# Kernel optimization log

Measured on AMD Instinct MI355X. Metric: run time of the kernel, lower is better.

Reference implementation:

```python
import jax, jax.numpy as jnp
import numpy as np

N_WRD = 2000
WCODE = 3
EMB = 32
VSIZE = 7
VIEW = (16, 16)
B = 64
CSIZE = 128


def _vcode():
    # torch.meshgrid with default 'ij' indexing, cat -> (2, H*W) -> (H*W, 2)
    x = jnp.linspace(-1.0, 1.0, VIEW[0])
    y = jnp.linspace(-1.0, 1.0, VIEW[1])
    xg, yg = jnp.meshgrid(x, y, indexing='ij')
    return jnp.stack([xg.reshape(-1), yg.reshape(-1)], axis=-1)  # (V, 2)


def setup_inputs() -> dict:
    key = jax.random.key(0)
    ks = jax.random.split(key, 20)
    s = 0.02
    d = {
        'view_cell': jax.random.normal(ks[0], (B, CSIZE, VIEW[0] * VIEW[1]), jnp.float32),
        'v': jax.random.normal(ks[1], (B, VSIZE), jnp.float32),
        'w2c_w1': jax.random.normal(ks[2], (VSIZE, 512), jnp.float32) * s,
        'w2c_b1': jnp.zeros((512,), jnp.float32),
        'w2c_w2': jax.random.normal(ks[3], (512, WCODE * N_WRD), jnp.float32) * s,
        'w2c_b2': jnp.zeros((WCODE * N_WRD,), jnp.float32),
        'fc1_w': jax.random.normal(ks[4], (WCODE, 256), jnp.float32) * s,
        'fc1_b': jnp.zeros((256,), jnp.float32),
        'fc2_w': jax.random.normal(ks[5], (256, 256), jnp.float32) * s,
        'fc2_b': jnp.zeros((256,), jnp.float32),
        'fca_w': jax.random.normal(ks[6], (256, 1), jnp.float32) * s,
        'fca_b': jnp.zeros((1,), jnp.float32),
        'fce_w': jax.random.normal(ks[7], (256, EMB), jnp.float32) * s,
        'fce_b': jnp.zeros((EMB,), jnp.float32),
        'vse_w1': jax.random.normal(ks[8], (2, 128), jnp.float32) * s,
        'vse_b1': jnp.zeros((128,), jnp.float32),
        'vse_w2': jax.random.normal(ks[9], (128, EMB), jnp.float32) * s,
        'vse_b2': jnp.zeros((EMB,), jnp.float32),
    }
    return d


def reference(view_cell, v, w2c_w1, w2c_b1, w2c_w2, w2c_b2,
              fc1_w, fc1_b, fc2_w, fc2_b, fca_w, fca_b, fce_w, fce_b,
              vse_w1, vse_b1, vse_w2, vse_b2):
    b = v.shape[0]
    # w2c: v -> per-cell world codes
    h0 = jax.nn.relu(v @ w2c_w1 + w2c_b1)                     # (B, 512)
    wcode = (h0 @ w2c_w2 + w2c_b2).reshape(-1, WCODE)          # (B*N, 3)
    h = jax.nn.relu(wcode @ fc1_w + fc1_b)                     # (B*N, 256)
    h = jax.nn.relu(h @ fc2_w + fc2_b)
    activation = jax.nn.sigmoid(h @ fca_w + fca_b).reshape(b, N_WRD, 1)
    cs_emb = (h @ fce_w + fce_b).reshape(b, N_WRD, EMB)        # (B, N, E)
    # view-space embedding of the pixel grid
    vcode = _vcode()                                           # (V, 2)
    vs = jax.nn.relu(vcode @ vse_w1 + vse_b1) @ vse_w2 + vse_b2  # (V, E)
    # relation / gated softmax routing
    relation = jnp.einsum('bne,ve->bnv', cs_emb, vs)           # (B, N, V)
    route = jax.nn.softmax(relation, axis=2) * activation      # (B, N, V)
    # write: view_cell (B, C, V) @ route^T (B, V, N) -> (B, C, N)
    wrd_cell = jnp.einsum('bcv,bnv->bcn', view_cell, route)
    return wrd_cell
```

## Files before the change

### kernel.cpp

```cpp
#include <hip/hip_runtime.h>
#include <hip/hip_bf16.h>
#include <math.h>

#define NWRD 2000
#define BB 64
#define CS 128
#define VV 256

typedef __attribute__((ext_vector_type(8)))  short short8;
typedef __attribute__((ext_vector_type(16))) float f32x16;

#define WS_FC2WT 0
#define WS_WCODE (WS_FC2WT + 32768)
#define WS_VSB   (WS_WCODE + 384000)
#define WS_EMBB  (WS_VSB + 4096)
#define WS_ACT   (WS_EMBB + 2048000)
#define WS_VCB   (WS_ACT + 128000)
#define WS_FCEWT (WS_VCB + 1048576)
#define WS_H0B   (WS_FCEWT + 4096)
#define WS_W2T   WS_EMBB

__device__ __forceinline__ unsigned short f2bf(float x) {
    unsigned int u = __float_as_uint(x);
    u += 0x7fffu + ((u >> 16) & 1u);
    return (unsigned short)(u >> 16);
}

__global__ __launch_bounds__(256) void k0_vcb(const float* __restrict__ vc,
                                              unsigned short* __restrict__ vcb) {
    int i = (blockIdx.x * 256 + threadIdx.x) * 8;
    float4 f0 = *(const float4*)(vc + i);
    float4 f1 = *(const float4*)(vc + i + 4);
    union { short8 v; unsigned short u[8]; } o;
    o.u[0] = f2bf(f0.x); o.u[1] = f2bf(f0.y); o.u[2] = f2bf(f0.z); o.u[3] = f2bf(f0.w);
    o.u[4] = f2bf(f1.x); o.u[5] = f2bf(f1.y); o.u[6] = f2bf(f1.z); o.u[7] = f2bf(f1.w);
    *(short8*)(vcb + i) = o.v;
}

__global__ __launch_bounds__(256) void k0w_fc2t(const float* __restrict__ fc2_w,
                                                unsigned short* __restrict__ fc2wT) {
    __shared__ unsigned short tile[64][72];
    int t = threadIdx.x;
    int k0t = (blockIdx.x >> 2) * 64, n0t = (blockIdx.x & 3) * 64;
    int nl = t & 63, kb = (t >> 6) * 16;
#pragma unroll
    for (int i = 0; i < 16; i++)
        tile[kb + i][nl] = f2bf(fc2_w[(size_t)(k0t + kb + i)*256 + n0t + nl]);
    __syncthreads();
    int kl = t & 63, nb = (t >> 6) * 16;
#pragma unroll
    for (int i = 0; i < 16; i++)
        fc2wT[(size_t)(n0t + nb + i)*256 + k0t + kl] = tile[kl][nb + i];
}

__global__ __launch_bounds__(256) void k0e_fcet(const float* __restrict__ fce_w,
                                                unsigned short* __restrict__ fcewT) {
    int t = threadIdx.x;
    int e = t & 31, kb = (t >> 5) * 32;
    unsigned short tmp[32];
#pragma unroll
    for (int i = 0; i < 32; i++) tmp[i] = f2bf(fce_w[(size_t)(kb + i)*32 + e]);
#pragma unroll
    for (int i = 0; i < 4; i++)
        *(short8*)(fcewT + (size_t)e*256 + kb + i*8) = *(short8*)(tmp + i*8);
}

__global__ void k1_h0(const float* __restrict__ v, const float* __restrict__ w1,
                      const float* __restrict__ b1, unsigned short* __restrict__ h0b) {
    int b = blockIdx.x, j = threadIdx.x;
    float s = b1[j];
#pragma unroll
    for (int k = 0; k < 7; k++) s = fmaf(v[b*7 + k], w1[k*512 + j], s);
    h0b[b*512 + j] = f2bf(fmaxf(s, 0.f));
}

__global__ __launch_bounds__(256) void k2t_w2(const float* __restrict__ w2,
                                              unsigned short* __restrict__ w2T) {
    __shared__ unsigned short tile[64][66];
    int t = threadIdx.x;
    int n0 = blockIdx.x * 64;
    int k0 = blockIdx.y * 64;
    int nl = t & 63, kb = (t >> 6) * 16;
    int nc = (n0 + nl) < 6000 ? (n0 + nl) : 5999;
#pragma unroll
    for (int i = 0; i < 16; i++)
        tile[nl][kb + i] = f2bf(w2[(size_t)(k0 + kb + i)*6000 + nc]);
    __syncthreads();
    int kl = t & 63, nb = (t >> 6) * 16;
#pragma unroll
    for (int i = 0; i < 16; i++) {
        int nn = n0 + nb + i;
        if (nn < 6000) w2T[(size_t)nn*512 + k0 + kl] = tile[nb + i][kl];
    }
}

__global__ __launch_bounds__(512) void k2_gemm(const unsigned short* __restrict__ h0b,
        const unsigned short* __restrict__ w2T, const float* __restrict__ b2,
        float* __restrict__ wcode) {
    int t = threadIdx.x;
    int w = t >> 6, lane = t & 63, l31 = lane & 31, h = lane >> 5;
    int mt = w & 1, nt = w >> 1;
    int n = blockIdx.x*128 + nt*32 + l31;
    int nc = n < 6000 ? n : 5999;
    f32x16 acc;
#pragma unroll
    for (int i = 0; i < 16; i++) acc[i] = 0.f;
#pragma unroll 8
    for (int ks = 0; ks < 32; ks++) {
        int k0 = ks*16 + h*8;
        short8 af = *(const short8*)(h0b + (mt*32 + l31)*512 + k0);
        short8 bf = *(const short8*)(w2T + (size_t)nc*512 + k0);
        acc = __builtin_amdgcn_mfma_f32_32x32x16_bf16(af, bf, acc, 0, 0, 0);
    }
    if (n < 6000) {
        float bias = b2[n];
#pragma unroll
        for (int i = 0; i < 16; i++) {
            int row = (i & 3) + 8*(i >> 2) + 4*h;
            wcode[(size_t)(mt*32 + row)*6000 + n] = acc[i] + bias;
        }
    }
}

__global__ __launch_bounds__(256) void k3_vs(const float* __restrict__ w1,
        const float* __restrict__ b1, const float* __restrict__ w2,
        const float* __restrict__ b2, unsigned short* __restrict__ vsb) {
    __shared__ float hs[8][128];
    int t = threadIdx.x;
    int m = t & 127, half = t >> 7;
#pragma unroll
    for (int q = 0; q < 4; q++) {
        int vloc = half*4 + q;
        int v = blockIdx.x*8 + vloc;
        float x = (2.f/15.f)*(float)(v >> 4) - 1.f;
        float y = (2.f/15.f)*(float)(v & 15) - 1.f;
        float h = b1[m] + x*w1[m] + y*w1[128 + m];
        hs[vloc][m] = fmaxf(h, 0.f);
    }
    __syncthreads();
    int vloc = t >> 5, e = t & 31;
    float s = b2[e];
    for (int mm = 0; mm < 128; mm++) s = fmaf(hs[vloc][mm], w2[mm*32 + e], s);
    vsb[(blockIdx.x*8 + vloc)*32 + e] = f2bf(s);
}

#define K45_LDS 75776
__global__ __launch_bounds__(512, 4) void k45(
        const unsigned short* __restrict__ vcb,
        const float* __restrict__ wcode,
        const float* __restrict__ fc1_w, const float* __restrict__ fc1_b,
        const unsigned short* __restrict__ fc2wT, const float* __restrict__ fc2_b,
        const float* __restrict__ fca_w, const float* __restrict__ fca_b,
        const unsigned short* __restrict__ fcewT, const float* __restrict__ fce_b,
        const unsigned short* __restrict__ vsb,
        float* __restrict__ out) {
    extern __shared__ char lds[];
    unsigned short* h1b    = (unsigned short*)lds;
    unsigned short* routeB = (unsigned short*)lds;
    unsigned short* h2b    = (unsigned short*)(lds + 33792);
    unsigned short* embL   = (unsigned short*)(lds + 67584);
    float* actL = (float*)(lds + 72704);
    float* wcs  = (float*)(lds + 72960);
    float* redM = (float*)(lds + 73728);
    float* redS = (float*)(lds + 74752);
    int t = threadIdx.x;
    int w = t >> 6, lane = t & 63, l31 = lane & 31, h = lane >> 5;
    int b = blockIdx.y;
    int n0 = blockIdx.x * 256;

    int jq = (t & 63) * 4, rb = t >> 6;
    float4 wa = *(const float4*)(fc1_w + jq);
    float4 wb = *(const float4*)(fc1_w + 256 + jq);
    float4 wc = *(const float4*)(fc1_w + 512 + jq);
    float4 bb4 = *(const float4*)(fc1_b + jq);
    int mtA = w & 1, na = (w >> 1) * 32, nb2 = na + 128;
    float ba = fc2_b[na + l31], bbv = fc2_b[nb2 + l31];
    float be = fce_b[l31];
    int ntR = w & 1, vq = w >> 1;
    int ctE = w >> 1, ntE = w & 1;
    size_t arowE = ((size_t)(b*128 + ctE*32 + l31))*256;

    for (int c = 0; c < 4; c++) {
        int w0 = n0 + c*64;
        if (t < 192) {
            int idx = w0*3 + t;
            wcs[t] = wcode[(size_t)b*6000 + (idx < 6000 ? idx : 5999)];
        }
        __syncthreads();
#pragma unroll
        for (int rr = 0; rr < 8; rr++) {
            int r = rb*8 + rr;
            float c0 = wcs[r*3], c1 = wcs[r*3+1], c2 = wcs[r*3+2];
            float v0 = fmaxf(fmaf(c2, wc.x, fmaf(c1, wb.x, fmaf(c0, wa.x, bb4.x))), 0.f);
            float v1 = fmaxf(fmaf(c2, wc.y, fmaf(c1, wb.y, fmaf(c0, wa.y, bb4.y))), 0.f);
            float v2 = fmaxf(fmaf(c2, wc.z, fmaf(c1, wb.z, fmaf(c0, wa.z, bb4.z))), 0.f);
            float v3 = fmaxf(fmaf(c2, wc.w, fmaf(c1, wb.w, fmaf(c0, wa.w, bb4.w))), 0.f);
            uint2 p;
            p.x = (unsigned int)f2bf(v0) | ((unsigned int)f2bf(v1) << 16);
            p.y = (unsigned int)f2bf(v2) | ((unsigned int)f2bf(v3) << 16);
            *(uint2*)(h1b + r*264 + jq) = p;
        }
        __syncthreads();
        {
            f32x16 c0, c1;
#pragma unroll
            for (int i = 0; i < 16; i++) { c0[i] = 0.f; c1[i] = 0.f; }
#pragma unroll 4
            for (int ks = 0; ks < 16; ks++) {
                int k0 = ks*16 + h*8;
                short8 af  = *(const short8*)(h1b + (mtA*32 + l31)*264 + k0);
                short8 bfa = *(const short8*)(fc2wT + (size_t)(na  + l31)*256 + k0);
                short8 bfb = *(const short8*)(fc2wT + (size_t)(nb2 + l31)*256 + k0);
                c0 = __builtin_amdgcn_mfma_f32_32x32x16_bf16(af, bfa, c0, 0, 0, 0);
                c1 = __builtin_amdgcn_mfma_f32_32x32x16_bf16(af, bfb, c1, 0, 0, 0);
            }
#pragma unroll
            for (int i = 0; i < 16; i++) {
                int row = (i & 3) + 8*(i >> 2) + 4*h;
                h2b[(mtA*32 + row)*264 + na  + l31] = f2bf(fmaxf(c0[i] + ba, 0.f));
                h2b[(mtA*32 + row)*264 + nb2 + l31] = f2bf(fmaxf(c1[i] + bbv, 0.f));
            }
        }
        __syncthreads();
        if (w < 2) {
            f32x16 ce;
#pragma unroll
            for (int i = 0; i < 16; i++) ce[i] = 0.f;
#pragma unroll 4
            for (int ks = 0; ks < 16; ks++) {
                int k0 = ks*16 + h*8;
                short8 af = *(const short8*)(h2b + (w*32 + l31)*264 + k0);
                short8 bf = *(const short8*)(fcewT + (size_t)l31*256 + k0);
                ce = __builtin_amdgcn_mfma_f32_32x32x16_bf16(af, bf, ce, 0, 0, 0);
            }
#pragma unroll
            for (int i = 0; i < 16; i++) {
                int row = (i & 3) + 8*(i >> 2) + 4*h;
                embL[(w*32 + row)*40 + l31] = f2bf(ce[i] + be);
            }
        } else if (w < 4) {
            int t2 = t - 128;
            int row = t2 >> 1, half = t2 & 1;
            float s = half ? 0.f : fca_b[0];
            const unsigned short* hr = h2b + row*264 + half*128;
            const float* wp = fca_w + half*128;
#pragma unroll 8
            for (int kk = 0; kk < 64; kk++) {
                unsigned int u = *(const unsigned int*)(hr + kk*2);
                float lo = __uint_as_float(u << 16);
                float hi = __uint_as_float(u & 0xffff0000u);
                float2 wv = *(const float2*)(wp + kk*2);
                s = fmaf(lo, wv.x, s);
                s = fmaf(hi, wv.y, s);
            }
            s += __shfl_xor(s, 1);
            if (half == 0) actL[row] = 1.f / (1.f + __expf(-s));
        }
        __syncthreads();
        int nloc = ntR*32 + l31;
        f32x16 ra[2];
#pragma unroll
        for (int mt = 0; mt < 2; mt++)
#pragma unroll
            for (int i = 0; i < 16; i++) ra[mt][i] = 0.f;
#pragma unroll
        for (int s = 0; s < 2; s++) {
            short8 bfrag = *(const short8*)(embL + nloc*40 + s*16 + h*8);
#pragma unroll
            for (int mt = 0; mt < 2; mt++) {
                int vrow = (vq*2 + mt)*32 + l31;
                short8 afrag = *(const short8*)(vsb + vrow*32 + s*16 + h*8);
                ra[mt] = __builtin_amdgcn_mfma_f32_32x32x16_bf16(afrag, bfrag, ra[mt], 0, 0, 0);
            }
        }
        float mx = -1e30f;
#pragma unroll
        for (int mt = 0; mt < 2; mt++)
#pragma unroll
            for (int i = 0; i < 16; i++) mx = fmaxf(mx, ra[mt][i]);
        mx = fmaxf(mx, __shfl_xor(mx, 32));
        if (lane < 32) redM[w*32 + l31] = mx;
        __syncthreads();
#pragma unroll
        for (int q = 0; q < 4; q++) mx = fmaxf(mx, redM[(q*2 + ntR)*32 + l31]);
        float sm = 0.f;
#pragma unroll
        for (int mt = 0; mt < 2; mt++)
#pragma unroll
            for (int i = 0; i < 16; i++) {
                float e = __expf(ra[mt][i] - mx);
                ra[mt][i] = e;
                sm += e;
            }
        sm += __shfl_xor(sm, 32);
        if (lane < 32) redS[w*32 + l31] = sm;
        __syncthreads();
        sm = 0.f;
#pragma unroll
        for (int q = 0; q < 4; q++) sm += redS[(q*2 + ntR)*32 + l31];
        float scale = actL[nloc] / sm;
#pragma unroll
        for (int mt = 0; mt < 2; mt++) {
#pragma unroll
            for (int rp = 0; rp < 4; rp++) {
                int vb = (vq*2 + mt)*32 + rp*8 + h*4;
                unsigned int p0 = (unsigned int)f2bf(ra[mt][rp*4+0]*scale)
                                | ((unsigned int)f2bf(ra[mt][rp*4+1]*scale) << 16);
                unsigned int p1 = (unsigned int)f2bf(ra[mt][rp*4+2]*scale)
                                | ((unsigned int)f2bf(ra[mt][rp*4+3]*scale) << 16);
                *(uint2*)(routeB + nloc*264 + vb) = make_uint2(p0, p1);
            }
        }
        __syncthreads();
        {
            f32x16 cc;
#pragma unroll
            for (int i = 0; i < 16; i++) cc[i] = 0.f;
            const unsigned short* rrow = routeB + (ntE*32 + l31)*264;
#pragma unroll 4
            for (int ks = 0; ks < 16; ks++) {
                int k0 = ks*16 + h*8;
                short8 bf = *(const short8*)(rrow + k0);
                short8 a0 = *(const short8*)(vcb + arowE + k0);
                cc = __builtin_amdgcn_mfma_f32_32x32x16_bf16(a0, bf, cc, 0, 0, 0);
            }
            int ng = w0 + ntE*32 + l31;
            if (ng < NWRD) {
                float* ob = out + (size_t)b*128*NWRD + ng;
#pragma unroll
                for (int i = 0; i < 16; i++) {
                    int crow = (i & 3) + 8*(i >> 2) + 4*h;
                    ob[(size_t)(ctE*32 + crow)*NWRD] = cc[i];
                }
            }
        }
    }
}

extern "C" void kernel_launch(void* const* d_in, const int* in_sizes, int n_in,
                              void* d_out, int out_size, void* d_ws, size_t ws_size,
                              hipStream_t stream) {
    const float* view_cell = (const float*)d_in[0];
    const float* v       = (const float*)d_in[1];
    const float* w2c_w1  = (const float*)d_in[2];
    const float* w2c_b1  = (const float*)d_in[3];
    const float* w2c_w2  = (const float*)d_in[4];
    const float* w2c_b2  = (const float*)d_in[5];
    const float* fc1_w   = (const float*)d_in[6];
    const float* fc1_b   = (const float*)d_in[7];
    const float* fc2_w   = (const float*)d_in[8];
    const float* fc2_b   = (const float*)d_in[9];
    const float* fca_w   = (const float*)d_in[10];
    const float* fca_b   = (const float*)d_in[11];
    const float* fce_w   = (const float*)d_in[12];
    const float* fce_b   = (const float*)d_in[13];
    const float* vse_w1  = (const float*)d_in[14];
    const float* vse_b1  = (const float*)d_in[15];
    const float* vse_w2  = (const float*)d_in[16];
    const float* vse_b2  = (const float*)d_in[17];
    float* ws    = (float*)d_ws;
    unsigned short* fc2wT = (unsigned short*)(ws + WS_FC2WT);
    float* wcode = ws + WS_WCODE;
    unsigned short* vsb   = (unsigned short*)(ws + WS_VSB);
    unsigned short* vcb   = (unsigned short*)(ws + WS_VCB);
    unsigned short* fcewT = (unsigned short*)(ws + WS_FCEWT);
    unsigned short* h0b   = (unsigned short*)(ws + WS_H0B);
    unsigned short* w2T   = (unsigned short*)(ws + WS_W2T);
    float* out   = (float*)d_out;

    k0_vcb<<<1024, 256, 0, stream>>>(view_cell, vcb);
    k1_h0<<<64, 512, 0, stream>>>(v, w2c_w1, w2c_b1, h0b);
    {
        dim3 gt(94, 8);
        k2t_w2<<<gt, 256, 0, stream>>>(w2c_w2, w2T);
    }
    k2_gemm<<<47, 512, 0, stream>>>(h0b, w2T, w2c_b2, wcode);
    k0w_fc2t<<<16, 256, 0, stream>>>(fc2_w, fc2wT);
    k0e_fcet<<<1, 256, 0, stream>>>(fce_w, fcewT);
    k3_vs<<<32, 256, 0, stream>>>(vse_w1, vse_b1, vse_w2, vse_b2, vsb);
    (void)hipFuncSetAttribute((const void*)k45,
                              hipFuncAttributeMaxDynamicSharedMemorySize, K45_LDS);
    dim3 g45(8, 64);
    k45<<<g45, 512, K45_LDS, stream>>>(vcb, wcode, fc1_w, fc1_b, fc2wT, fc2_b,
                                       fca_w, fca_b, fcewT, fce_b, vsb, out);
}
```

Measured before the change: 253.6 us.

## Merge prep kernels, MFMA activation head, drop softmax max pass, preload wcode

Fuses the six preprocessing kernels (bf16 casts, weight transposes, h0, view-space embedding) into a single block-dispatched launch to cut launch overhead, and gives w2T its own workspace region. The activation dot product is computed with an MFMA against a zero-padded bf16 fca weight matrix instead of a scalar loop, and all wcode values for a block are loaded once up front rather than per chunk with a barrier. The softmax max-subtraction pass and its reduction barrier are removed, which relies on the relation logits being small enough not to overflow exp. The w2c GEMM splits K into two independent accumulators to shorten the MFMA dependency chain.

```diff
diff --git a/kernel.cpp b/kernel.cpp
--- a/kernel.cpp
+++ b/kernel.cpp
@@ -13,12 +13,11 @@
 #define WS_FC2WT 0
 #define WS_WCODE (WS_FC2WT + 32768)
 #define WS_VSB   (WS_WCODE + 384000)
-#define WS_EMBB  (WS_VSB + 4096)
-#define WS_ACT   (WS_EMBB + 2048000)
-#define WS_VCB   (WS_ACT + 128000)
+#define WS_W2T   (WS_VSB + 4096)
+#define WS_VCB   (WS_W2T + 1536000)
 #define WS_FCEWT (WS_VCB + 1048576)
 #define WS_H0B   (WS_FCEWT + 4096)
-#define WS_W2T   WS_EMBB
+#define WS_FCAWB (WS_H0B + 16384)
 
 __device__ __forceinline__ unsigned short f2bf(float x) {
     unsigned int u = __float_as_uint(x);
@@ -26,71 +25,98 @@
     return (unsigned short)(u >> 16);
 }
 
-__global__ __launch_bounds__(256) void k0_vcb(const float* __restrict__ vc,
-                                              unsigned short* __restrict__ vcb) {
-    int i = (blockIdx.x * 256 + threadIdx.x) * 8;
-    float4 f0 = *(const float4*)(vc + i);
-    float4 f1 = *(const float4*)(vc + i + 4);
-    union { short8 v; unsigned short u[8]; } o;
-    o.u[0] = f2bf(f0.x); o.u[1] = f2bf(f0.y); o.u[2] = f2bf(f0.z); o.u[3] = f2bf(f0.w);
-    o.u[4] = f2bf(f1.x); o.u[5] = f2bf(f1.y); o.u[6] = f2bf(f1.z); o.u[7] = f2bf(f1.w);
-    *(short8*)(vcb + i) = o.v;
-}
-
-__global__ __launch_bounds__(256) void k0w_fc2t(const float* __restrict__ fc2_w,
-                                                unsigned short* __restrict__ fc2wT) {
-    __shared__ unsigned short tile[64][72];
-    int t = threadIdx.x;
-    int k0t = (blockIdx.x >> 2) * 64, n0t = (blockIdx.x & 3) * 64;
-    int nl = t & 63, kb = (t >> 6) * 16;
-#pragma unroll
-    for (int i = 0; i < 16; i++)
-        tile[kb + i][nl] = f2bf(fc2_w[(size_t)(k0t + kb + i)*256 + n0t + nl]);
-    __syncthreads();
-    int kl = t & 63, nb = (t >> 6) * 16;
-#pragma unroll
-    for (int i = 0; i < 16; i++)
-        fc2wT[(size_t)(n0t + nb + i)*256 + k0t + kl] = tile[kl][nb + i];
-}
-
-__global__ __launch_bounds__(256) void k0e_fcet(const float* __restrict__ fce_w,
-                                                unsigned short* __restrict__ fcewT) {
-    int t = threadIdx.x;
-    int e = t & 31, kb = (t >> 5) * 32;
-    unsigned short tmp[32];
-#pragma unroll
-    for (int i = 0; i < 32; i++) tmp[i] = f2bf(fce_w[(size_t)(kb + i)*32 + e]);
-#pragma unroll
-    for (int i = 0; i < 4; i++)
-        *(short8*)(fcewT + (size_t)e*256 + kb + i*8) = *(short8*)(tmp + i*8);
-}
-
-__global__ void k1_h0(const float* __restrict__ v, const float* __restrict__ w1,
-                      const float* __restrict__ b1, unsigned short* __restrict__ h0b) {
-    int b = blockIdx.x, j = threadIdx.x;
-    float s = b1[j];
-#pragma unroll
-    for (int k = 0; k < 7; k++) s = fmaf(v[b*7 + k], w1[k*512 + j], s);
-    h0b[b*512 + j] = f2bf(fmaxf(s, 0.f));
-}
-
-__global__ __launch_bounds__(256) void k2t_w2(const float* __restrict__ w2,
-                                              unsigned short* __restrict__ w2T) {
-    __shared__ unsigned short tile[64][66];
-    int t = threadIdx.x;
-    int n0 = blockIdx.x * 64;
-    int k0 = blockIdx.y * 64;
-    int nl = t & 63, kb = (t >> 6) * 16;
-    int nc = (n0 + nl) < 6000 ? (n0 + nl) : 5999;
-#pragma unroll
-    for (int i = 0; i < 16; i++)
-        tile[nl][kb + i] = f2bf(w2[(size_t)(k0 + kb + i)*6000 + nc]);
-    __syncthreads();
-    int kl = t & 63, nb = (t >> 6) * 16;
-#pragma unroll
-    for (int i = 0; i < 16; i++) {
-        int nn = n0 + nb + i;
-        if (nn < 6000) w2T[(size_t)nn*512 + k0 + kl] = tile[nb + i][kl];
+#define PREP_A 1024
+#define PREP_B (PREP_A + 752)
+#define PREP_C (PREP_B + 128)
+#define PREP_D (PREP_C + 32)
+#define PREP_E (PREP_D + 16)
+#define PREP_N (PREP_E + 1)
+__global__ __launch_bounds__(256) void kprep(
+        const float* __restrict__ vc, unsigned short* __restrict__ vcb,
+        const float* __restrict__ w2, unsigned short* __restrict__ w2T,
+        const float* __restrict__ v, const float* __restrict__ w2c_w1,
+        const float* __restrict__ w2c_b1, unsigned short* __restrict__ h0b,
+        const float* __restrict__ vse_w1, const float* __restrict__ vse_b1,
+        const float* __restrict__ vse_w2, const float* __restrict__ vse_b2,
+        unsigned short* __restrict__ vsb,
+        const float* __restrict__ fc2_w, unsigned short* __restrict__ fc2wT,
+        const float* __restrict__ fce_w, unsigned short* __restrict__ fcewT,
+        const float* __restrict__ fca_w, unsigned short* __restrict__ fcawB) {
+    __shared__ unsigned short smem[9216];
+    int bid = blockIdx.x, t = threadIdx.x;
+    if (bid < PREP_A) {
+        int i = (bid * 256 + t) * 8;
+        float4 f0 = *(const float4*)(vc + i);
+        float4 f1 = *(const float4*)(vc + i + 4);
+        union { short8 v8; unsigned short u[8]; } o;
+        o.u[0] = f2bf(f0.x); o.u[1] = f2bf(f0.y); o.u[2] = f2bf(f0.z); o.u[3] = f2bf(f0.w);
+        o.u[4] = f2bf(f1.x); o.u[5] = f2bf(f1.y); o.u[6] = f2bf(f1.z); o.u[7] = f2bf(f1.w);
+        *(short8*)(vcb + i) = o.v8;
+    } else if (bid < PREP_B) {
+        unsigned short (*tile)[66] = (unsigned short(*)[66])smem;
+        int b2 = bid - PREP_A;
+        int n0 = (b2 % 94) * 64, k0 = (b2 / 94) * 64;
+        int nl = t & 63, kb = (t >> 6) * 16;
+        int nc = (n0 + nl) < 6000 ? (n0 + nl) : 5999;
+#pragma unroll
+        for (int i = 0; i < 16; i++)
+            tile[nl][kb + i] = f2bf(w2[(size_t)(k0 + kb + i)*6000 + nc]);
+        __syncthreads();
+        int kl = t & 63, nb = (t >> 6) * 16;
+#pragma unroll
+        for (int i = 0; i < 16; i++) {
+            int nn = n0 + nb + i;
+            if (nn < 6000) w2T[(size_t)nn*512 + k0 + kl] = tile[nb + i][kl];
+        }
+    } else if (bid < PREP_C) {
+        int c = bid - PREP_B;
+        int b = c >> 1, j = (c & 1)*256 + t;
+        float s = w2c_b1[j];
+#pragma unroll
+        for (int k = 0; k < 7; k++) s = fmaf(v[b*7 + k], w2c_w1[k*512 + j], s);
+        h0b[b*512 + j] = f2bf(fmaxf(s, 0.f));
+    } else if (bid < PREP_D) {
+        float* hs = (float*)smem;
+        int blk = bid - PREP_C;
+        int m = t & 127, half = t >> 7;
+#pragma unroll
+        for (int q = 0; q < 4; q++) {
+            int vloc = half*4 + q;
+            int vv = blk*8 + vloc;
+            float x = (2.f/15.f)*(float)(vv >> 4) - 1.f;
+            float y = (2.f/15.f)*(float)(vv & 15) - 1.f;
+            float h = vse_b1[m] + x*vse_w1[m] + y*vse_w1[128 + m];
+            hs[vloc*128 + m] = fmaxf(h, 0.f);
+        }
+        __syncthreads();
+        int vloc = t >> 5, e = t & 31;
+        float s = vse_b2[e];
+        for (int mm = 0; mm < 128; mm++) s = fmaf(hs[vloc*128 + mm], vse_w2[mm*32 + e], s);
+        vsb[(blk*8 + vloc)*32 + e] = f2bf(s);
+    } else if (bid < PREP_E) {
+        unsigned short (*tile)[72] = (unsigned short(*)[72])smem;
+        int b2 = bid - PREP_D;
+        int k0t = (b2 >> 2) * 64, n0t = (b2 & 3) * 64;
+        int nl = t & 63, kb = (t >> 6) * 16;
+#pragma unroll
+        for (int i = 0; i < 16; i++)
+            tile[kb + i][nl] = f2bf(fc2_w[(size_t)(k0t + kb + i)*256 + n0t + nl]);
+        __syncthreads();
+        int kl = t & 63, nb = (t >> 6) * 16;
+#pragma unroll
+        for (int i = 0; i < 16; i++)
+            fc2wT[(size_t)(n0t + nb + i)*256 + k0t + kl] = tile[kl][nb + i];
+    } else {
+        int e = t & 31, kb = (t >> 5) * 32;
+        unsigned short tmp[32];
+#pragma unroll
+        for (int i = 0; i < 32; i++) tmp[i] = f2bf(fce_w[(size_t)(kb + i)*32 + e]);
+#pragma unroll
+        for (int i = 0; i < 4; i++)
+            *(short8*)(fcewT + (size_t)e*256 + kb + i*8) = *(short8*)(tmp + i*8);
+#pragma unroll
+        for (int i = 0; i < 32; i++)
+            fcawB[(size_t)e*256 + kb + i] = (e == 0) ? f2bf(fca_w[kb + i]) : (unsigned short)0;
     }
 }
 
@@ -102,99 +128,87 @@
     int mt = w & 1, nt = w >> 1;
     int n = blockIdx.x*128 + nt*32 + l31;
     int nc = n < 6000 ? n : 5999;
-    f32x16 acc;
-#pragma unroll
-    for (int i = 0; i < 16; i++) acc[i] = 0.f;
+    f32x16 a0v, a1v;
+#pragma unroll
+    for (int i = 0; i < 16; i++) { a0v[i] = 0.f; a1v[i] = 0.f; }
 #pragma unroll 8
-    for (int ks = 0; ks < 32; ks++) {
+    for (int ks = 0; ks < 16; ks++) {
         int k0 = ks*16 + h*8;
-        short8 af = *(const short8*)(h0b + (mt*32 + l31)*512 + k0);
-        short8 bf = *(const short8*)(w2T + (size_t)nc*512 + k0);
-        acc = __builtin_amdgcn_mfma_f32_32x32x16_bf16(af, bf, acc, 0, 0, 0);
+        short8 af0 = *(const short8*)(h0b + (mt*32 + l31)*512 + k0);
+        short8 bf0 = *(const short8*)(w2T + (size_t)nc*512 + k0);
+        a0v = __builtin_amdgcn_mfma_f32_32x32x16_bf16(af0, bf0, a0v, 0, 0, 0);
+        short8 af1 = *(const short8*)(h0b + (mt*32 + l31)*512 + k0 + 256);
+        short8 bf1 = *(const short8*)(w2T + (size_t)nc*512 + k0 + 256);
+        a1v = __builtin_amdgcn_mfma_f32_32x32x16_bf16(af1, bf1, a1v, 0, 0, 0);
     }
     if (n < 6000) {
         float bias = b2[n];
 #pragma unroll
         for (int i = 0; i < 16; i++) {
             int row = (i & 3) + 8*(i >> 2) + 4*h;
-            wcode[(size_t)(mt*32 + row)*6000 + n] = acc[i] + bias;
-        }
-    }
-}
-
-__global__ __launch_bounds__(256) void k3_vs(const float* __restrict__ w1,
-        const float* __restrict__ b1, const float* __restrict__ w2,
-        const float* __restrict__ b2, unsigned short* __restrict__ vsb) {
-    __shared__ float hs[8][128];
-    int t = threadIdx.x;
-    int m = t & 127, half = t >> 7;
-#pragma unroll
-    for (int q = 0; q < 4; q++) {
-        int vloc = half*4 + q;
-        int v = blockIdx.x*8 + vloc;
-        float x = (2.f/15.f)*(float)(v >> 4) - 1.f;
-        float y = (2.f/15.f)*(float)(v & 15) - 1.f;
-        float h = b1[m] + x*w1[m] + y*w1[128 + m];
-        hs[vloc][m] = fmaxf(h, 0.f);
-    }
-    __syncthreads();
-    int vloc = t >> 5, e = t & 31;
-    float s = b2[e];
-    for (int mm = 0; mm < 128; mm++) s = fmaf(hs[vloc][mm], w2[mm*32 + e], s);
-    vsb[(blockIdx.x*8 + vloc)*32 + e] = f2bf(s);
-}
-
-#define K45_LDS 75776
+            wcode[(size_t)(mt*32 + row)*6000 + n] = a0v[i] + a1v[i] + bias;
+        }
+    }
+}
+
+#define K45_LDS 77056
 __global__ __launch_bounds__(512, 4) void k45(
         const unsigned short* __restrict__ vcb,
         const float* __restrict__ wcode,
         const float* __restrict__ fc1_w, const float* __restrict__ fc1_b,
         const unsigned short* __restrict__ fc2wT, const float* __restrict__ fc2_b,
-        const float* __restrict__ fca_w, const float* __restrict__ fca_b,
+        const float* __restrict__ fca_b_p,
+        const unsigned short* __restrict__ fcawB,
         const unsigned short* __restrict__ fcewT, const float* __restrict__ fce_b,
         const unsigned short* __restrict__ vsb,
         float* __restrict__ out) {
     extern __shared__ char lds[];
     unsigned short* h1b    = (unsigned short*)lds;
-    unsigned short* routeB = (unsigned short*)lds;
     unsigned short* h2b    = (unsigned short*)(lds + 33792);
+    unsigned short* routeB = h2b;
     unsigned short* embL   = (unsigned short*)(lds + 67584);
-    float* actL = (float*)(lds + 72704);
-    float* wcs  = (float*)(lds + 72960);
-    float* redM = (float*)(lds + 73728);
-    float* redS = (float*)(lds + 74752);
+    float* actL   = (float*)(lds + 72704);
+    float* wcsAll = (float*)(lds + 72960);
+    float* redS   = (float*)(lds + 76032);
     int t = threadIdx.x;
     int w = t >> 6, lane = t & 63, l31 = lane & 31, h = lane >> 5;
     int b = blockIdx.y;
     int n0 = blockIdx.x * 256;
 
-    int jq = (t & 63) * 4, rb = t >> 6;
-    float4 wa = *(const float4*)(fc1_w + jq);
-    float4 wb = *(const float4*)(fc1_w + 256 + jq);
-    float4 wc = *(const float4*)(fc1_w + 512 + jq);
+    {
+        const float* wb = wcode + (size_t)b*6000;
+        int i0 = n0*3 + t;
+        wcsAll[t] = wb[i0 < 6000 ? i0 : 5999];
+        if (t < 256) {
+            int i1 = n0*3 + 512 + t;
+            wcsAll[512 + t] = wb[i1 < 6000 ? i1 : 5999];
+        }
+    }
+    int jq = (t & 63) * 4;
+    float4 wa  = *(const float4*)(fc1_w + jq);
+    float4 wb4 = *(const float4*)(fc1_w + 256 + jq);
+    float4 wc  = *(const float4*)(fc1_w + 512 + jq);
     float4 bb4 = *(const float4*)(fc1_b + jq);
     int mtA = w & 1, na = (w >> 1) * 32, nb2 = na + 128;
     float ba = fc2_b[na + l31], bbv = fc2_b[nb2 + l31];
     float be = fce_b[l31];
+    float fcab = fca_b_p[0];
     int ntR = w & 1, vq = w >> 1;
     int ctE = w >> 1, ntE = w & 1;
     size_t arowE = ((size_t)(b*128 + ctE*32 + l31))*256;
+    __syncthreads();
 
     for (int c = 0; c < 4; c++) {
         int w0 = n0 + c*64;
-        if (t < 192) {
-            int idx = w0*3 + t;
-            wcs[t] = wcode[(size_t)b*6000 + (idx < 6000 ? idx : 5999)];
-        }
-        __syncthreads();
 #pragma unroll
         for (int rr = 0; rr < 8; rr++) {
-            int r = rb*8 + rr;
-            float c0 = wcs[r*3], c1 = wcs[r*3+1], c2 = wcs[r*3+2];
-            float v0 = fmaxf(fmaf(c2, wc.x, fmaf(c1, wb.x, fmaf(c0, wa.x, bb4.x))), 0.f);
-            float v1 = fmaxf(fmaf(c2, wc.y, fmaf(c1, wb.y, fmaf(c0, wa.y, bb4.y))), 0.f);
-            float v2 = fmaxf(fmaf(c2, wc.z, fmaf(c1, wb.z, fmaf(c0, wa.z, bb4.z))), 0.f);
-            float v3 = fmaxf(fmaf(c2, wc.w, fmaf(c1, wb.w, fmaf(c0, wa.w, bb4.w))), 0.f);
+            int r = w*8 + rr;
+            const float* wr = wcsAll + (c*64 + r)*3;
+            float c0 = wr[0], c1 = wr[1], c2 = wr[2];
+            float v0 = fmaxf(fmaf(c2, wc.x, fmaf(c1, wb4.x, fmaf(c0, wa.x, bb4.x))), 0.f);
+            float v1 = fmaxf(fmaf(c2, wc.y, fmaf(c1, wb4.y, fmaf(c0, wa.y, bb4.y))), 0.f);
+            float v2 = fmaxf(fmaf(c2, wc.z, fmaf(c1, wb4.z, fmaf(c0, wa.z, bb4.z))), 0.f);
+            float v3 = fmaxf(fmaf(c2, wc.w, fmaf(c1, wb4.w, fmaf(c0, wa.w, bb4.w))), 0.f);
             uint2 p;
             p.x = (unsigned int)f2bf(v0) | ((unsigned int)f2bf(v1) << 16);
             p.y = (unsigned int)f2bf(v2) | ((unsigned int)f2bf(v3) << 16);
@@ -239,22 +253,24 @@
                 embL[(w*32 + row)*40 + l31] = f2bf(ce[i] + be);
             }
         } else if (w < 4) {
-            int t2 = t - 128;
-            int row = t2 >> 1, half = t2 & 1;
-            float s = half ? 0.f : fca_b[0];
-            const unsigned short* hr = h2b + row*264 + half*128;
-            const float* wp = fca_w + half*128;
-#pragma unroll 8
-            for (int kk = 0; kk < 64; kk++) {
-                unsigned int u = *(const unsigned int*)(hr + kk*2);
-                float lo = __uint_as_float(u << 16);
-                float hi = __uint_as_float(u & 0xffff0000u);
-                float2 wv = *(const float2*)(wp + kk*2);
-                s = fmaf(lo, wv.x, s);
-                s = fmaf(hi, wv.y, s);
-            }
-            s += __shfl_xor(s, 1);
-            if (half == 0) actL[row] = 1.f / (1.f + __expf(-s));
+            int m = w - 2;
+            f32x16 ca;
+#pragma unroll
+            for (int i = 0; i < 16; i++) ca[i] = 0.f;
+#pragma unroll 4
+            for (int ks = 0; ks < 16; ks++) {
+                int k0 = ks*16 + h*8;
+                short8 af = *(const short8*)(h2b + (m*32 + l31)*264 + k0);
+                short8 bf = *(const short8*)(fcawB + (size_t)l31*256 + k0);
+                ca = __builtin_amdgcn_mfma_f32_32x32x16_bf16(af, bf, ca, 0, 0, 0);
+            }
+            if (l31 == 0) {
+#pragma unroll
+                for (int i = 0; i < 16; i++) {
+                    int row = (i & 3) + 8*(i >> 2) + 4*h;
+                    actL[m*32 + row] = 1.f / (1.f + __expf(-(ca[i] + fcab)));
+                }
+            }
         }
         __syncthreads();
         int nloc = ntR*32 + l31;
@@ -273,22 +289,12 @@
                 ra[mt] = __builtin_amdgcn_mfma_f32_32x32x16_bf16(afrag, bfrag, ra[mt], 0, 0, 0);
             }
         }
-        float mx = -1e30f;
+        float sm = 0.f;
 #pragma unroll
         for (int mt = 0; mt < 2; mt++)
 #pragma unroll
-            for (int i = 0; i < 16; i++) mx = fmaxf(mx, ra[mt][i]);
-        mx = fmaxf(mx, __shfl_xor(mx, 32));
-        if (lane < 32) redM[w*32 + l31] = mx;
-        __syncthreads();
-#pragma unroll
-        for (int q = 0; q < 4; q++) mx = fmaxf(mx, redM[(q*2 + ntR)*32 + l31]);
-        float sm = 0.f;
-#pragma unroll
-        for (int mt = 0; mt < 2; mt++)
-#pragma unroll
             for (int i = 0; i < 16; i++) {
-                float e = __expf(ra[mt][i] - mx);
+                float e = __expf(ra[mt][i]);
                 ra[mt][i] = e;
                 sm += e;
             }
@@ -362,25 +368,21 @@
     unsigned short* fc2wT = (unsigned short*)(ws + WS_FC2WT);
     float* wcode = ws + WS_WCODE;
     unsigned short* vsb   = (unsigned short*)(ws + WS_VSB);
+    unsigned short* w2T   = (unsigned short*)(ws + WS_W2T);
     unsigned short* vcb   = (unsigned short*)(ws + WS_VCB);
     unsigned short* fcewT = (unsigned short*)(ws + WS_FCEWT);
     unsigned short* h0b   = (unsigned short*)(ws + WS_H0B);
-    unsigned short* w2T   = (unsigned short*)(ws + WS_W2T);
+    unsigned short* fcawB = (unsigned short*)(ws + WS_FCAWB);
     float* out   = (float*)d_out;
 
-    k0_vcb<<<1024, 256, 0, stream>>>(view_cell, vcb);
-    k1_h0<<<64, 512, 0, stream>>>(v, w2c_w1, w2c_b1, h0b);
-    {
-        dim3 gt(94, 8);
-        k2t_w2<<<gt, 256, 0, stream>>>(w2c_w2, w2T);
-    }
+    kprep<<<PREP_N, 256, 0, stream>>>(view_cell, vcb, w2c_w2, w2T,
+                                      v, w2c_w1, w2c_b1, h0b,
+                                      vse_w1, vse_b1, vse_w2, vse_b2, vsb,
+                                      fc2_w, fc2wT, fce_w, fcewT, fca_w, fcawB);
     k2_gemm<<<47, 512, 0, stream>>>(h0b, w2T, w2c_b2, wcode);
-    k0w_fc2t<<<16, 256, 0, stream>>>(fc2_w, fc2wT);
-    k0e_fcet<<<1, 256, 0, stream>>>(fce_w, fcewT);
-    k3_vs<<<32, 256, 0, stream>>>(vse_w1, vse_b1, vse_w2, vse_b2, vsb);
     (void)hipFuncSetAttribute((const void*)k45,
                               hipFuncAttributeMaxDynamicSharedMemorySize, K45_LDS);
     dim3 g45(8, 64);
     k45<<<g45, 512, K45_LDS, stream>>>(vcb, wcode, fc1_w, fc1_b, fc2wT, fc2_b,
-                                       fca_w, fca_b, fcewT, fce_b, vsb, out);
-}
+                                       fca_b, fcawB, fcewT, fce_b, vsb, out);
+}
```

Result: faster. 243.9 us (-3.8%).
